# Kernel tuning notes

Measured on AMD Instinct MI355X. Metric: run time of the kernel, lower is better.

## Reference

```python
import jax, jax.numpy as jnp
import numpy as np

# binarize = sign() in forward; standard BNN binarize uses a straight-through
# estimator (gradient clipped to |x|<=1) in backward. Forward math: sign.

def binarize(x):
    return jnp.sign(x)


def setup_inputs() -> dict:
    key = jax.random.key(0)
    k1, k2 = jax.random.split(key)
    M, K, N = 8192, 4096, 4096
    x = jax.random.normal(k1, (M, K), dtype=jnp.float32)
    # xavier-scale init for weight; scale is irrelevant after sign() but kept realistic
    w = jax.random.normal(k2, (K, N), dtype=jnp.float32) * np.sqrt(2.0 / (K + N)).astype(np.float32)
    return {"x": x, "weight": w}


def reference(x, weight):
    # sign-binarize activations and weights, then dense matmul
    xb = binarize(x)            # [M, K] in {-1, 0, +1}
    wb = binarize(weight)       # [K, N]
    return jnp.matmul(xb, wb)   # [M, N]
```

## Files before the change

kernel.cpp:

```cpp
#include <hip/hip_runtime.h>
#include <stdint.h>

#define M_DIM 8192
#define K_DIM 4096
#define N_DIM 4096

using i32x4 = __attribute__((ext_vector_type(4))) int;
using i32x8 = __attribute__((ext_vector_type(8))) int;
using f32x16 = __attribute__((ext_vector_type(16))) float;

typedef const __attribute__((address_space(1))) void g_void;
typedef __attribute__((address_space(3))) void lds_void;

__device__ __forceinline__ void gload_lds16(const void* g, void* l) {
  __builtin_amdgcn_global_load_lds((g_void*)g, (lds_void*)l, 16, 0, 0);
}

__device__ __forceinline__ void barrier_raw() {
  asm volatile("" ::: "memory");
  __builtin_amdgcn_s_barrier();
  asm volatile("" ::: "memory");
}

__device__ __forceinline__ unsigned code4(float v) {
  return v > 0.f ? 0x2u : (v < 0.f ? 0xAu : 0x0u);
}

__global__ void pack_x4_kernel(const float* __restrict__ in,
                               uint8_t* __restrict__ out) {
  __shared__ __align__(16) uint16_t cds[32 * 264];
  int g = blockIdx.x;
  int tq = blockIdx.y;
  int tid = threadIdx.x;
#pragma unroll
  for (int i = 0; i < 32; ++i) {
    int flat = tid + 256 * i;
    int row = flat >> 8;
    int c4 = flat & 255;
    const float4 v = *reinterpret_cast<const float4*>(
        in + (long)(g * 32 + row) * K_DIM + tq * 1024 + c4 * 4);
    unsigned u = code4(v.x) | (code4(v.y) << 4) | (code4(v.z) << 8) |
                 (code4(v.w) << 12);
    cds[row * 264 + c4] = (uint16_t)u;
  }
  __syncthreads();
#pragma unroll
  for (int j = 0; j < 4; ++j) {
    int u = tid + 256 * j;
    int tl = u >> 7;
    int kc = (u >> 5) & 3;
    int row = u & 31;
    i32x4 val = *reinterpret_cast<const i32x4*>(&cds[row * 264 + tl * 32 + kc * 8]);
    int t = tq * 8 + tl;
    long o = ((((long)g * 32 + t) * 4 + kc) * 32 + row) * 16;
    *reinterpret_cast<i32x4*>(out + o) = val;
  }
}

__global__ void pack_wt4_kernel(const float* __restrict__ w,
                                uint8_t* __restrict__ out) {
  __shared__ __align__(16) uint8_t tile[64 * 144];
  int n0 = blockIdx.x * 64;
  int k0 = blockIdx.y * 128;
  int tid = threadIdx.x;
#pragma unroll
  for (int i = 0; i < 32; ++i) {
    int flat = tid + 256 * i;
    int r = flat >> 6;
    int c = flat & 63;
    tile[c * 144 + r] = (uint8_t)code4(w[(long)(k0 + r) * N_DIM + n0 + c]);
  }
  __syncthreads();
  int rg = tid >> 7, kc = (tid >> 5) & 3, row = tid & 31;
  const unsigned* sp =
      reinterpret_cast<const unsigned*>(&tile[(rg * 32 + row) * 144 + kc * 32]);
  i32x4 val;
#pragma unroll
  for (int d = 0; d < 4; ++d) {
    unsigned s0 = sp[2 * d], s1 = sp[2 * d + 1];
    unsigned t0 = s0 & 0x0F0F0F0Fu, t1 = s1 & 0x0F0F0F0Fu;
    unsigned p = (t0 | (t0 >> 4)) & 0x00FF00FFu;
    unsigned q = (t1 | (t1 >> 4)) & 0x00FF00FFu;
    val[d] = (int)((p & 0xFFu) | ((p >> 8) & 0xFF00u) | ((q & 0xFFu) << 16) |
                   ((q >> 16) << 24));
  }
  int g = (n0 >> 5) + rg;
  int t = k0 >> 7;
  long o = ((((long)g * 32 + t) * 4 + kc) * 32 + row) * 16;
  *reinterpret_cast<i32x4*>(out + o) = val;
}

__device__ __forceinline__ i32x8 lo8(i32x4 r) {
  return __builtin_shufflevector(r, r, 0, 1, 2, 3, -1, -1, -1, -1);
}

#define SCALE1 0x7f7f7f7f

template <int VM, bool ISSUE, int CUR>
__device__ __forceinline__ void tile_step(
    int t, const uint8_t* __restrict__ gA, const uint8_t* __restrict__ gB,
    int dstA, uint8_t* lds, int aRd, i32x4 (&bC)[4], i32x4 (&bN)[4],
    f32x16 (&acc)[4][2]) {
  const uint8_t* buf = lds + CUR * 8192;
  if (ISSUE) {
    long kn = (long)(t + 2) * 2048;
    bN[0] = *reinterpret_cast<const i32x4*>(gB + kn);
    bN[1] = *reinterpret_cast<const i32x4*>(gB + 65536 + kn);
    bN[2] = *reinterpret_cast<const i32x4*>(gB + kn + 1024);
    bN[3] = *reinterpret_cast<const i32x4*>(gB + 65536 + kn + 1024);
    uint8_t* nbuf = lds + ((CUR + 2) % 3) * 8192;
    gload_lds16(gA + kn, nbuf + dstA);
    gload_lds16(gA + kn + 1024, nbuf + dstA + 1024);
  }
  i32x4 a0[4], a1[4];
#pragma unroll
  for (int mi = 0; mi < 4; ++mi)
    a0[mi] = *reinterpret_cast<const i32x4*>(buf + aRd + mi * 2048);
#pragma unroll
  for (int mi = 0; mi < 4; ++mi)
    a1[mi] = *reinterpret_cast<const i32x4*>(buf + aRd + mi * 2048 + 1024);
  asm volatile("s_waitcnt lgkmcnt(4)" ::: "memory");
  __builtin_amdgcn_sched_barrier(0);
  __builtin_amdgcn_s_setprio(1);
#pragma unroll
  for (int mi = 0; mi < 4; ++mi)
#pragma unroll
    for (int ni = 0; ni < 2; ++ni)
      acc[mi][ni] = __builtin_amdgcn_mfma_scale_f32_32x32x64_f8f6f4(
          lo8(a0[mi]), lo8(bC[ni]), acc[mi][ni], 4, 4, 0, SCALE1, 0, SCALE1);
  __builtin_amdgcn_s_setprio(0);
  asm volatile("s_waitcnt lgkmcnt(0)" ::: "memory");
  __builtin_amdgcn_sched_barrier(0);
  __builtin_amdgcn_s_setprio(1);
#pragma unroll
  for (int mi = 0; mi < 4; ++mi)
#pragma unroll
    for (int ni = 0; ni < 2; ++ni)
      acc[mi][ni] = __builtin_amdgcn_mfma_scale_f32_32x32x64_f8f6f4(
          lo8(a1[mi]), lo8(bC[2 + ni]), acc[mi][ni], 4, 4, 0, SCALE1, 0,
          SCALE1);
  __builtin_amdgcn_s_setprio(0);
  if (VM >= 0) {
    if (VM == 6) asm volatile("s_waitcnt vmcnt(6)" ::: "memory");
    else asm volatile("s_waitcnt vmcnt(0)" ::: "memory");
    barrier_raw();
  }
}

__global__ __launch_bounds__(256, 2) void gemm_fp4_kernel(
    const uint8_t* __restrict__ A, const uint8_t* __restrict__ B,
    float* __restrict__ C) {
  __shared__ __align__(16) uint8_t lds[3 * 8192];

  int bid = blockIdx.x;
  int xcd = bid & 7;
  int i = bid >> 3;
  int bn = (i & 7) + ((xcd & 1) << 3);
  int bm = (i >> 3) + ((xcd >> 1) << 4);

  int tid = threadIdx.x;
  int wid = tid >> 6;
  int lane = tid & 63;

  const uint8_t* gA = A + (long)(bm * 4 + wid) * 65536 + lane * 16;
  const uint8_t* gB = B + (long)(bn * 8 + 2 * wid) * 65536 + lane * 16;
  int dstA = wid * 2048;

  int aRd = lane * 16;

  i32x4 bs0[4], bs1[4], bs2[4];
  f32x16 acc[4][2] = {};

  bs0[0] = *reinterpret_cast<const i32x4*>(gB);
  bs0[1] = *reinterpret_cast<const i32x4*>(gB + 65536);
  bs0[2] = *reinterpret_cast<const i32x4*>(gB + 1024);
  bs0[3] = *reinterpret_cast<const i32x4*>(gB + 65536 + 1024);
  gload_lds16(gA, lds + dstA);
  gload_lds16(gA + 1024, lds + dstA + 1024);
  bs1[0] = *reinterpret_cast<const i32x4*>(gB + 2048);
  bs1[1] = *reinterpret_cast<const i32x4*>(gB + 65536 + 2048);
  bs1[2] = *reinterpret_cast<const i32x4*>(gB + 3072);
  bs1[3] = *reinterpret_cast<const i32x4*>(gB + 65536 + 3072);
  gload_lds16(gA + 2048, lds + 8192 + dstA);
  gload_lds16(gA + 3072, lds + 8192 + dstA + 1024);
  asm volatile("s_waitcnt vmcnt(6)" ::: "memory");
  barrier_raw();

#pragma unroll 1
  for (int tt = 0; tt < 30; tt += 3) {
    tile_step<6, true, 0>(tt, gA, gB, dstA, lds, aRd, bs0, bs2, acc);
    tile_step<6, true, 1>(tt + 1, gA, gB, dstA, lds, aRd, bs1, bs0, acc);
    tile_step<6, true, 2>(tt + 2, gA, gB, dstA, lds, aRd, bs2, bs1, acc);
  }
  tile_step<0, false, 0>(30, gA, gB, dstA, lds, aRd, bs0, bs2, acc);
  tile_step<-1, false, 1>(31, gA, gB, dstA, lds, aRd, bs1, bs0, acc);

  long row0 = (long)bm * 128 + ((lane >> 5) << 2);
  long col0 = (long)bn * 256 + wid * 64 + (lane & 31);
#pragma unroll
  for (int mi = 0; mi < 4; ++mi)
#pragma unroll
    for (int ni = 0; ni < 2; ++ni)
#pragma unroll
      for (int r = 0; r < 16; ++r) {
        long row = row0 + mi * 32 + (r & 3) + ((r >> 2) << 3);
        C[row * N_DIM + col0 + ni * 32] = acc[mi][ni][r];
      }
}

extern "C" void kernel_launch(void* const* d_in, const int* in_sizes, int n_in,
                              void* d_out, int out_size, void* d_ws, size_t ws_size,
                              hipStream_t stream) {
  const float* x = (const float*)d_in[0];
  const float* w = (const float*)d_in[1];
  float* out = (float*)d_out;

  uint8_t* x4 = (uint8_t*)d_ws;
  uint8_t* w4t = x4 + (size_t)M_DIM * (K_DIM / 2);

  pack_x4_kernel<<<dim3(M_DIM / 32, 4), 256, 0, stream>>>(x, x4);
  pack_wt4_kernel<<<dim3(N_DIM / 64, K_DIM / 128), 256, 0, stream>>>(w, w4t);
  gemm_fp4_kernel<<<1024, 256, 0, stream>>>(x4, w4t, out);
}
```

Baseline: 125.4 us.

## Process two K-tiles per barrier with four-slot LDS ring

```diff
diff --git a/kernel.cpp b/kernel.cpp
--- a/kernel.cpp
+++ b/kernel.cpp
@@ -96,53 +96,66 @@
 
 #define SCALE1 0x7f7f7f7f
 
-template <int VM, bool ISSUE, int CUR>
-__device__ __forceinline__ void tile_step(
+#define MFMA8(AV, BV0, BV1)                                                 \
+  do {                                                                      \
+    __builtin_amdgcn_sched_barrier(0);                                      \
+    __builtin_amdgcn_s_setprio(1);                                          \
+    _Pragma("unroll") for (int mi = 0; mi < 4; ++mi) {                      \
+      acc[mi][0] = __builtin_amdgcn_mfma_scale_f32_32x32x64_f8f6f4(         \
+          lo8(AV[mi]), lo8(BV0), acc[mi][0], 4, 4, 0, SCALE1, 0, SCALE1);   \
+      acc[mi][1] = __builtin_amdgcn_mfma_scale_f32_32x32x64_f8f6f4(         \
+          lo8(AV[mi]), lo8(BV1), acc[mi][1], 4, 4, 0, SCALE1, 0, SCALE1);   \
+    }                                                                       \
+    __builtin_amdgcn_s_setprio(0);                                          \
+  } while (0)
+
+template <bool ISSUE, bool GATE, int CUR>
+__device__ __forceinline__ void pair_step(
     int t, const uint8_t* __restrict__ gA, const uint8_t* __restrict__ gB,
-    int dstA, uint8_t* lds, int aRd, i32x4 (&bC)[4], i32x4 (&bN)[4],
-    f32x16 (&acc)[4][2]) {
-  const uint8_t* buf = lds + CUR * 8192;
+    int dstA, uint8_t* lds, int aRd, i32x4 (&bC0)[4], i32x4 (&bC1)[4],
+    i32x4 (&bN0)[4], i32x4 (&bN1)[4], f32x16 (&acc)[4][2]) {
   if (ISSUE) {
-    long kn = (long)(t + 2) * 2048;
-    bN[0] = *reinterpret_cast<const i32x4*>(gB + kn);
-    bN[1] = *reinterpret_cast<const i32x4*>(gB + 65536 + kn);
-    bN[2] = *reinterpret_cast<const i32x4*>(gB + kn + 1024);
-    bN[3] = *reinterpret_cast<const i32x4*>(gB + 65536 + kn + 1024);
-    uint8_t* nbuf = lds + ((CUR + 2) % 3) * 8192;
-    gload_lds16(gA + kn, nbuf + dstA);
-    gload_lds16(gA + kn + 1024, nbuf + dstA + 1024);
-  }
-  i32x4 a0[4], a1[4];
-#pragma unroll
-  for (int mi = 0; mi < 4; ++mi)
-    a0[mi] = *reinterpret_cast<const i32x4*>(buf + aRd + mi * 2048);
-#pragma unroll
-  for (int mi = 0; mi < 4; ++mi)
-    a1[mi] = *reinterpret_cast<const i32x4*>(buf + aRd + mi * 2048 + 1024);
+    long k2 = (long)(t + 2) * 2048, k3 = (long)(t + 3) * 2048;
+    bN0[0] = *reinterpret_cast<const i32x4*>(gB + k2);
+    bN0[1] = *reinterpret_cast<const i32x4*>(gB + 65536 + k2);
+    bN0[2] = *reinterpret_cast<const i32x4*>(gB + k2 + 1024);
+    bN0[3] = *reinterpret_cast<const i32x4*>(gB + 65536 + k2 + 1024);
+    bN1[0] = *reinterpret_cast<const i32x4*>(gB + k3);
+    bN1[1] = *reinterpret_cast<const i32x4*>(gB + 65536 + k3);
+    bN1[2] = *reinterpret_cast<const i32x4*>(gB + k3 + 1024);
+    bN1[3] = *reinterpret_cast<const i32x4*>(gB + 65536 + k3 + 1024);
+    uint8_t* nb0 = lds + ((CUR + 2) & 3) * 8192;
+    uint8_t* nb1 = lds + ((CUR + 3) & 3) * 8192;
+    gload_lds16(gA + k2, nb0 + dstA);
+    gload_lds16(gA + k2 + 1024, nb0 + dstA + 1024);
+    gload_lds16(gA + k3, nb1 + dstA);
+    gload_lds16(gA + k3 + 1024, nb1 + dstA + 1024);
+  }
+  const uint8_t* buf0 = lds + CUR * 8192;
+  const uint8_t* buf1 = lds + ((CUR + 1) & 3) * 8192;
+  i32x4 a0[4], a1[4], c0[4], c1[4];
+#pragma unroll
+  for (int mi = 0; mi < 4; ++mi)
+    a0[mi] = *reinterpret_cast<const i32x4*>(buf0 + aRd + mi * 2048);
+#pragma unroll
+  for (int mi = 0; mi < 4; ++mi)
+    a1[mi] = *reinterpret_cast<const i32x4*>(buf0 + aRd + mi * 2048 + 1024);
   asm volatile("s_waitcnt lgkmcnt(4)" ::: "memory");
-  __builtin_amdgcn_sched_barrier(0);
-  __builtin_amdgcn_s_setprio(1);
-#pragma unroll
-  for (int mi = 0; mi < 4; ++mi)
-#pragma unroll
-    for (int ni = 0; ni < 2; ++ni)
-      acc[mi][ni] = __builtin_amdgcn_mfma_scale_f32_32x32x64_f8f6f4(
-          lo8(a0[mi]), lo8(bC[ni]), acc[mi][ni], 4, 4, 0, SCALE1, 0, SCALE1);
-  __builtin_amdgcn_s_setprio(0);
+  MFMA8(a0, bC0[0], bC0[1]);
+#pragma unroll
+  for (int mi = 0; mi < 4; ++mi)
+    c0[mi] = *reinterpret_cast<const i32x4*>(buf1 + aRd + mi * 2048);
+#pragma unroll
+  for (int mi = 0; mi < 4; ++mi)
+    c1[mi] = *reinterpret_cast<const i32x4*>(buf1 + aRd + mi * 2048 + 1024);
+  asm volatile("s_waitcnt lgkmcnt(8)" ::: "memory");
+  MFMA8(a1, bC0[2], bC0[3]);
+  asm volatile("s_waitcnt lgkmcnt(4)" ::: "memory");
+  MFMA8(c0, bC1[0], bC1[1]);
   asm volatile("s_waitcnt lgkmcnt(0)" ::: "memory");
-  __builtin_amdgcn_sched_barrier(0);
-  __builtin_amdgcn_s_setprio(1);
-#pragma unroll
-  for (int mi = 0; mi < 4; ++mi)
-#pragma unroll
-    for (int ni = 0; ni < 2; ++ni)
-      acc[mi][ni] = __builtin_amdgcn_mfma_scale_f32_32x32x64_f8f6f4(
-          lo8(a1[mi]), lo8(bC[2 + ni]), acc[mi][ni], 4, 4, 0, SCALE1, 0,
-          SCALE1);
-  __builtin_amdgcn_s_setprio(0);
-  if (VM >= 0) {
-    if (VM == 6) asm volatile("s_waitcnt vmcnt(6)" ::: "memory");
-    else asm volatile("s_waitcnt vmcnt(0)" ::: "memory");
+  MFMA8(c1, bC1[2], bC1[3]);
+  if (GATE) {
+    asm volatile("s_waitcnt vmcnt(0)" ::: "memory");
     barrier_raw();
   }
 }
@@ -150,7 +163,7 @@
 __global__ __launch_bounds__(256, 2) void gemm_fp4_kernel(
     const uint8_t* __restrict__ A, const uint8_t* __restrict__ B,
     float* __restrict__ C) {
-  __shared__ __align__(16) uint8_t lds[3 * 8192];
+  __shared__ __align__(16) uint8_t lds[4 * 8192];
 
   int bid = blockIdx.x;
   int xcd = bid & 7;
@@ -165,35 +178,34 @@
   const uint8_t* gA = A + (long)(bm * 4 + wid) * 65536 + lane * 16;
   const uint8_t* gB = B + (long)(bn * 8 + 2 * wid) * 65536 + lane * 16;
   int dstA = wid * 2048;
-
   int aRd = lane * 16;
 
-  i32x4 bs0[4], bs1[4], bs2[4];
+  i32x4 bsA[4], bsB[4], bsC[4], bsD[4];
   f32x16 acc[4][2] = {};
 
-  bs0[0] = *reinterpret_cast<const i32x4*>(gB);
-  bs0[1] = *reinterpret_cast<const i32x4*>(gB + 65536);
-  bs0[2] = *reinterpret_cast<const i32x4*>(gB + 1024);
-  bs0[3] = *reinterpret_cast<const i32x4*>(gB + 65536 + 1024);
+  bsA[0] = *reinterpret_cast<const i32x4*>(gB);
+  bsA[1] = *reinterpret_cast<const i32x4*>(gB + 65536);
+  bsA[2] = *reinterpret_cast<const i32x4*>(gB + 1024);
+  bsA[3] = *reinterpret_cast<const i32x4*>(gB + 65536 + 1024);
+  bsB[0] = *reinterpret_cast<const i32x4*>(gB + 2048);
+  bsB[1] = *reinterpret_cast<const i32x4*>(gB + 65536 + 2048);
+  bsB[2] = *reinterpret_cast<const i32x4*>(gB + 3072);
+  bsB[3] = *reinterpret_cast<const i32x4*>(gB + 65536 + 3072);
   gload_lds16(gA, lds + dstA);
   gload_lds16(gA + 1024, lds + dstA + 1024);
-  bs1[0] = *reinterpret_cast<const i32x4*>(gB + 2048);
-  bs1[1] = *reinterpret_cast<const i32x4*>(gB + 65536 + 2048);
-  bs1[2] = *reinterpret_cast<const i32x4*>(gB + 3072);
-  bs1[3] = *reinterpret_cast<const i32x4*>(gB + 65536 + 3072);
   gload_lds16(gA + 2048, lds + 8192 + dstA);
   gload_lds16(gA + 3072, lds + 8192 + dstA + 1024);
-  asm volatile("s_waitcnt vmcnt(6)" ::: "memory");
+  asm volatile("s_waitcnt vmcnt(0)" ::: "memory");
   barrier_raw();
 
 #pragma unroll 1
-  for (int tt = 0; tt < 30; tt += 3) {
-    tile_step<6, true, 0>(tt, gA, gB, dstA, lds, aRd, bs0, bs2, acc);
-    tile_step<6, true, 1>(tt + 1, gA, gB, dstA, lds, aRd, bs1, bs0, acc);
-    tile_step<6, true, 2>(tt + 2, gA, gB, dstA, lds, aRd, bs2, bs1, acc);
-  }
-  tile_step<0, false, 0>(30, gA, gB, dstA, lds, aRd, bs0, bs2, acc);
-  tile_step<-1, false, 1>(31, gA, gB, dstA, lds, aRd, bs1, bs0, acc);
+  for (int k = 0; k < 7; ++k) {
+    int t = k * 4;
+    pair_step<true, true, 0>(t, gA, gB, dstA, lds, aRd, bsA, bsB, bsC, bsD, acc);
+    pair_step<true, true, 2>(t + 2, gA, gB, dstA, lds, aRd, bsC, bsD, bsA, bsB, acc);
+  }
+  pair_step<true, true, 0>(28, gA, gB, dstA, lds, aRd, bsA, bsB, bsC, bsD, acc);
+  pair_step<false, false, 2>(30, gA, gB, dstA, lds, aRd, bsC, bsD, bsA, bsB, acc);
 
   long row0 = (long)bm * 128 + ((lane >> 5) << 2);
   long col0 = (long)bn * 256 + wid * 64 + (lane & 31);
```

Result: slower. 129.4 us (+3.2%).
